# Optimization experiments

Hardware: AMD Instinct MI355X
Metric: run time of the kernel (lower is better)

The kernel has to match this reference:

```python
import jax, jax.numpy as jnp
import numpy as np

N = 100000      # node_size
R = 2000        # rel_size
E = 300000      # triple_size == nnz(adj)
ER = 300000     # nnz of node-to-rel adjacency
EE = 300000     # nnz of node-to-node adjacency
NODE_F = 128
REL_F = 128
ENT_F = NODE_F + REL_F  # 256
DEPTH = 2


def setup_inputs() -> dict:
    key = jax.random.key(0)
    ks = jax.random.split(key, 14)
    return {
        'ent_emb': jax.random.normal(ks[0], (N, NODE_F), jnp.float32) * 0.1,
        'rel_emb': jax.random.normal(ks[1], (R, REL_F), jnp.float32) * 0.1,
        'a_self': jax.random.normal(ks[2], (ENT_F, 1), jnp.float32) * 0.1,
        'a_neigh': jax.random.normal(ks[3], (ENT_F, 1), jnp.float32) * 0.1,
        'a_rel': jax.random.normal(ks[4], (REL_F, 1), jnp.float32) * 0.1,
        'sp_val': jax.random.uniform(ks[5], (E,), jnp.float32),
        'adj_row': jax.random.randint(ks[6], (E,), 0, N),
        'adj_col': jax.random.randint(ks[7], (E,), 0, N),
        'sp_row': jnp.arange(E),
        'sp_col': jax.random.randint(ks[8], (E,), 0, R),
        'rel_row': jax.random.randint(ks[9], (ER,), 0, N),
        'rel_col': jax.random.randint(ks[10], (ER,), 0, R),
        'ent_row': jax.random.randint(ks[11], (EE,), 0, N),
        'ent_col': jax.random.randint(ks[12], (EE,), 0, N),
    }


def _mean_agg(row, col, emb, nrows):
    # tf.sparse_softmax over all-ones values == 1/deg per row -> row mean
    deg = jax.ops.segment_sum(jnp.ones(row.shape, emb.dtype), row, nrows)
    w = 1.0 / deg[row]
    return jax.ops.segment_sum(w[:, None] * emb[col], row, nrows)


def _segment_softmax(vals, seg, nseg):
    m = jax.ops.segment_max(vals, seg, nseg)
    e = jnp.exp(vals - m[seg])
    s = jax.ops.segment_sum(e, seg, nseg)
    return e / s[seg]


def reference(ent_emb, rel_emb, a_self, a_neigh, a_rel, sp_val,
              adj_row, adj_col, sp_row, sp_col, rel_row, rel_col, ent_row, ent_col):
    # initial features: mean-aggregated entity + relation features
    rel_feat = _mean_agg(rel_row, rel_col, rel_emb, N)
    ent_feat = _mean_agg(ent_row, ent_col, ent_emb, N)
    features = jax.nn.relu(jnp.concatenate([ent_feat, rel_feat], axis=-1))  # [N, ENT_F]
    outputs = [features]

    # per-edge relation attention term: (T,R) sparse @ (rel_emb @ a_rel); constant across depth
    rel_proj = (rel_emb @ a_rel)[:, 0]                               # [R]
    rel_attn = jax.ops.segment_sum(sp_val * rel_proj[sp_col], sp_row, E)  # [E]

    att = None
    for _ in range(DEPTH):
        a_s = (features @ a_self)[:, 0]    # [N]
        a_n = (features @ a_neigh)[:, 0]   # [N]
        att = rel_attn + a_s[adj_row] + a_n[adj_col]          # [E]
        att = jax.nn.leaky_relu(att, negative_slope=0.2)
        att = _segment_softmax(att, adj_row, N)               # row-wise sparse softmax
        features = jax.nn.relu(
            jax.ops.segment_sum(att[:, None] * features[adj_col], adj_row, N))
        outputs.append(features)

    out = jnp.concatenate(outputs, axis=-1)  # [N, ENT_F*(DEPTH+1)]
    return out, att
```

## Files before the change

### kernel.cpp

```cpp
#include <hip/hip_runtime.h>

#define NODE_F 128
#define ENT_F  256
#define LDO    768
#define NEG_INF -3.4e38f


__global__ void count3_k(const int* __restrict__ r0, const int* __restrict__ r1,
                         const int* __restrict__ r2, int E0, int E1, int E2,
                         int* __restrict__ deg3, int N) {
    int i = blockIdx.x * blockDim.x + threadIdx.x;
    int y = blockIdx.y;
    const int* rp = (y == 0) ? r0 : (y == 1) ? r1 : r2;
    int Eg = (y == 0) ? E0 : (y == 1) ? E1 : E2;
    if (i < Eg) atomicAdd(&deg3[(size_t)y * N + rp[i]], 1);
}

__global__ void alloc3_k(const int* __restrict__ deg3, int* __restrict__ tot3,
                         int* __restrict__ start3, int* __restrict__ cur3, int N) {
    int y = blockIdx.y;
    int i = blockIdx.x * blockDim.x + threadIdx.x;
    int lane = threadIdx.x & 63;
    int d = (i < N) ? deg3[(size_t)y * N + i] : 0;
    int v = d;
    #pragma unroll
    for (int o = 1; o < 64; o <<= 1) {
        int t = __shfl_up(v, o);
        if (lane >= o) v += t;
    }
    int wsum = __shfl(v, 63);
    int base = 0;
    if (lane == 63) base = atomicAdd(&tot3[y], wsum);
    base = __shfl(base, 63);
    if (i < N) {
        int st = base + v - d;
        start3[(size_t)y * N + i] = st;
        cur3[(size_t)y * N + i] = st;
    }
}

__global__ void scatter3_k(const int* __restrict__ r0, const int* __restrict__ c0,
                           const int* __restrict__ r1, const int* __restrict__ c1,
                           const int* __restrict__ r2, const int* __restrict__ c2,
                           int E0, int E1, int E2, int* __restrict__ cur3,
                           int* __restrict__ col_adj, int* __restrict__ eid_adj,
                           int* __restrict__ col_ent, int* __restrict__ col_rel,
                           const float* __restrict__ sp_val, const int* __restrict__ sp_col,
                           const float* __restrict__ proj, float* __restrict__ rel_attn_s,
                           int N) {
    int e = blockIdx.x * blockDim.x + threadIdx.x;
    int y = blockIdx.y;
    const int* rp = (y == 0) ? r0 : (y == 1) ? r1 : r2;
    const int* cp = (y == 0) ? c0 : (y == 1) ? c1 : c2;
    int* colp = (y == 0) ? col_adj : (y == 1) ? col_ent : col_rel;
    int Eg = (y == 0) ? E0 : (y == 1) ? E1 : E2;
    if (e >= Eg) return;
    int r = rp[e];
    int pos = atomicAdd(&cur3[(size_t)y * N + r], 1);
    colp[pos] = cp[e];
    if (y == 0) {
        eid_adj[pos] = e;
        rel_attn_s[pos] = sp_val[e] * proj[sp_col[e]];
    }
}

__global__ void rel_proj_k(const float* __restrict__ rel_emb, const float* __restrict__ a_rel,
                           float* __restrict__ proj, int R) {
    int r = blockIdx.x * blockDim.x + threadIdx.x;
    if (r >= R) return;
    float s = 0.0f;
    #pragma unroll 4
    for (int f = 0; f < NODE_F; ++f) s += rel_emb[(size_t)r * NODE_F + f] * a_rel[f];
    proj[r] = s;
}


__global__ void meanagg_fused_k(const int* __restrict__ st_ent, const int* __restrict__ dg_ent,
                                const int* __restrict__ col_ent,
                                const int* __restrict__ st_rel, const int* __restrict__ dg_rel,
                                const int* __restrict__ col_rel,
                                const float* __restrict__ ent_emb, const float* __restrict__ rel_emb,
                                const float* __restrict__ a_self, const float* __restrict__ a_neigh,
                                float* __restrict__ out,
                                float* __restrict__ a_s_out, float* __restrict__ a_n_out, int N) {
    int n = blockIdx.x * (blockDim.x >> 6) + (threadIdx.x >> 6);
    int lane = threadIdx.x & 63;
    if (n >= N) return;

    float2 ea = {0.0f, 0.0f};
    {
        int s = st_ent[n], deg = dg_ent[n];
        int p = 0;
        for (; p + 4 <= deg; p += 4) {
            int c0 = col_ent[s + p], c1 = col_ent[s + p + 1];
            int c2 = col_ent[s + p + 2], c3 = col_ent[s + p + 3];
            float2 v0 = reinterpret_cast<const float2*>(&ent_emb[(size_t)c0 * NODE_F])[lane];
            float2 v1 = reinterpret_cast<const float2*>(&ent_emb[(size_t)c1 * NODE_F])[lane];
            float2 v2 = reinterpret_cast<const float2*>(&ent_emb[(size_t)c2 * NODE_F])[lane];
            float2 v3 = reinterpret_cast<const float2*>(&ent_emb[(size_t)c3 * NODE_F])[lane];
            ea.x += v0.x + v1.x + v2.x + v3.x;
            ea.y += v0.y + v1.y + v2.y + v3.y;
        }
        for (; p < deg; ++p) {
            float2 v = reinterpret_cast<const float2*>(&ent_emb[(size_t)col_ent[s + p] * NODE_F])[lane];
            ea.x += v.x; ea.y += v.y;
        }
        if (deg > 0) { float w = 1.0f / (float)deg; ea.x *= w; ea.y *= w; }
    }

    float2 ra = {0.0f, 0.0f};
    {
        int s = st_rel[n], deg = dg_rel[n];
        int p = 0;
        for (; p + 4 <= deg; p += 4) {
            int c0 = col_rel[s + p], c1 = col_rel[s + p + 1];
            int c2 = col_rel[s + p + 2], c3 = col_rel[s + p + 3];
            float2 v0 = reinterpret_cast<const float2*>(&rel_emb[(size_t)c0 * NODE_F])[lane];
            float2 v1 = reinterpret_cast<const float2*>(&rel_emb[(size_t)c1 * NODE_F])[lane];
            float2 v2 = reinterpret_cast<const float2*>(&rel_emb[(size_t)c2 * NODE_F])[lane];
            float2 v3 = reinterpret_cast<const float2*>(&rel_emb[(size_t)c3 * NODE_F])[lane];
            ra.x += v0.x + v1.x + v2.x + v3.x;
            ra.y += v0.y + v1.y + v2.y + v3.y;
        }
        for (; p < deg; ++p) {
            float2 v = reinterpret_cast<const float2*>(&rel_emb[(size_t)col_rel[s + p] * NODE_F])[lane];
            ra.x += v.x; ra.y += v.y;
        }
        if (deg > 0) { float w = 1.0f / (float)deg; ra.x *= w; ra.y *= w; }
    }

    ea.x = ea.x > 0.0f ? ea.x : 0.0f;  ea.y = ea.y > 0.0f ? ea.y : 0.0f;
    ra.x = ra.x > 0.0f ? ra.x : 0.0f;  ra.y = ra.y > 0.0f ? ra.y : 0.0f;

    reinterpret_cast<float2*>(&out[(size_t)n * LDO])[lane] = ea;
    reinterpret_cast<float2*>(&out[(size_t)n * LDO + NODE_F])[lane] = ra;

    float2 se = reinterpret_cast<const float2*>(a_self)[lane];
    float2 sr = reinterpret_cast<const float2*>(a_self)[64 + lane];
    float2 ne = reinterpret_cast<const float2*>(a_neigh)[lane];
    float2 nr = reinterpret_cast<const float2*>(a_neigh)[64 + lane];
    float ds = ea.x * se.x + ea.y * se.y + ra.x * sr.x + ra.y * sr.y;
    float dn = ea.x * ne.x + ea.y * ne.y + ra.x * nr.x + ra.y * nr.y;
    #pragma unroll
    for (int o = 32; o > 0; o >>= 1) {
        ds += __shfl_xor(ds, o);
        dn += __shfl_xor(dn, o);
    }
    if (lane == 0) { a_s_out[n] = ds; a_n_out[n] = dn; }
}

__global__ void attn_agg_fused_k(const int* __restrict__ st, const int* __restrict__ dg,
                                 const int* __restrict__ col_s, const int* __restrict__ eid_s,
                                 const float* __restrict__ rel_attn_s,
                                 const float* __restrict__ a_s_in, const float* __restrict__ a_n_in,
                                 const float* __restrict__ a_self, const float* __restrict__ a_neigh,
                                 float* __restrict__ a_s_out, float* __restrict__ a_n_out,
                                 float* __restrict__ out, int src, int dst,
                                 float* __restrict__ att_out, int N) {
    int n = blockIdx.x * (blockDim.x >> 6) + (threadIdx.x >> 6);
    int lane = threadIdx.x & 63;
    if (n >= N) return;
    int s = st[n];
    int deg = dg[n];
    float4 acc = {0.0f, 0.0f, 0.0f, 0.0f};

    if (deg > 0) {
        float as_row = a_s_in[n];
        if (deg <= 64) {
            float myv = NEG_INF;
            int mycol = 0;
            if (lane < deg) {
                int p = s + lane;
                mycol = col_s[p];
                float v = rel_attn_s[p] + as_row + a_n_in[mycol];
                myv = v >= 0.0f ? v : 0.2f * v;
            }
            float m = myv;
            #pragma unroll
            for (int o = 32; o > 0; o >>= 1) {
                float x = __shfl_xor(m, o);
                m = x > m ? x : m;
            }
            float ex = (lane < deg) ? __expf(myv - m) : 0.0f;
            float ssum = ex;
            #pragma unroll
            for (int o = 32; o > 0; o >>= 1) ssum += __shfl_xor(ssum, o);
            float myatt = ex / ssum;
            if (att_out && lane < deg) att_out[eid_s[s + lane]] = myatt;

            int p = 0;
            for (; p + 4 <= deg; p += 4) {
                float a0 = __shfl(myatt, p),     a1 = __shfl(myatt, p + 1);
                float a2 = __shfl(myatt, p + 2), a3 = __shfl(myatt, p + 3);
                int c0 = __shfl(mycol, p),     c1 = __shfl(mycol, p + 1);
                int c2 = __shfl(mycol, p + 2), c3 = __shfl(mycol, p + 3);
                float4 v0 = reinterpret_cast<const float4*>(&out[(size_t)c0 * LDO + src])[lane];
                float4 v1 = reinterpret_cast<const float4*>(&out[(size_t)c1 * LDO + src])[lane];
                float4 v2 = reinterpret_cast<const float4*>(&out[(size_t)c2 * LDO + src])[lane];
                float4 v3 = reinterpret_cast<const float4*>(&out[(size_t)c3 * LDO + src])[lane];
                acc.x += a0 * v0.x + a1 * v1.x + a2 * v2.x + a3 * v3.x;
                acc.y += a0 * v0.y + a1 * v1.y + a2 * v2.y + a3 * v3.y;
                acc.z += a0 * v0.z + a1 * v1.z + a2 * v2.z + a3 * v3.z;
                acc.w += a0 * v0.w + a1 * v1.w + a2 * v2.w + a3 * v3.w;
            }
            for (; p < deg; ++p) {
                float a = __shfl(myatt, p);
                int c = __shfl(mycol, p);
                float4 v = reinterpret_cast<const float4*>(&out[(size_t)c * LDO + src])[lane];
                acc.x += a * v.x; acc.y += a * v.y; acc.z += a * v.z; acc.w += a * v.w;
            }
        } else {
            float m = NEG_INF;
            for (int p = s + lane; p < s + deg; p += 64) {
                float v = rel_attn_s[p] + as_row + a_n_in[col_s[p]];
                v = v >= 0.0f ? v : 0.2f * v;
                m = v > m ? v : m;
            }
            #pragma unroll
            for (int o = 32; o > 0; o >>= 1) {
                float x = __shfl_xor(m, o);
                m = x > m ? x : m;
            }
            float ssum = 0.0f;
            for (int p = s + lane; p < s + deg; p += 64) {
                float v = rel_attn_s[p] + as_row + a_n_in[col_s[p]];
                v = v >= 0.0f ? v : 0.2f * v;
                ssum += __expf(v - m);
            }
            #pragma unroll
            for (int o = 32; o > 0; o >>= 1) ssum += __shfl_xor(ssum, o);
            float inv = 1.0f / ssum;
            for (int p = s; p < s + deg; ++p) {
                int c = col_s[p];
                float v = rel_attn_s[p] + as_row + a_n_in[c];
                v = v >= 0.0f ? v : 0.2f * v;
                float a = __expf(v - m) * inv;
                if (att_out && lane == 0) att_out[eid_s[p]] = a;
                float4 fv = reinterpret_cast<const float4*>(&out[(size_t)c * LDO + src])[lane];
                acc.x += a * fv.x; acc.y += a * fv.y; acc.z += a * fv.z; acc.w += a * fv.w;
            }
        }
    }

    acc.x = acc.x > 0.0f ? acc.x : 0.0f;
    acc.y = acc.y > 0.0f ? acc.y : 0.0f;
    acc.z = acc.z > 0.0f ? acc.z : 0.0f;
    acc.w = acc.w > 0.0f ? acc.w : 0.0f;
    reinterpret_cast<float4*>(&out[(size_t)n * LDO + dst])[lane] = acc;

    if (a_s_out) {
        float4 s4 = reinterpret_cast<const float4*>(a_self)[lane];
        float4 n4 = reinterpret_cast<const float4*>(a_neigh)[lane];
        float ds = acc.x * s4.x + acc.y * s4.y + acc.z * s4.z + acc.w * s4.w;
        float dn = acc.x * n4.x + acc.y * n4.y + acc.z * n4.z + acc.w * n4.w;
        #pragma unroll
        for (int o = 32; o > 0; o >>= 1) {
            ds += __shfl_xor(ds, o);
            dn += __shfl_xor(dn, o);
        }
        if (lane == 0) { a_s_out[n] = ds; a_n_out[n] = dn; }
    }
}


extern "C" void kernel_launch(void* const* d_in, const int* in_sizes, int n_in,
                              void* d_out, int out_size, void* d_ws, size_t ws_size,
                              hipStream_t stream) {
    const float* ent_emb = (const float*)d_in[0];
    const float* rel_emb = (const float*)d_in[1];
    const float* a_self  = (const float*)d_in[2];
    const float* a_neigh = (const float*)d_in[3];
    const float* a_rel   = (const float*)d_in[4];
    const float* sp_val  = (const float*)d_in[5];
    const int*   adj_row = (const int*)d_in[6];
    const int*   adj_col = (const int*)d_in[7];
    const int*   sp_col  = (const int*)d_in[9];
    const int*   rel_row = (const int*)d_in[10];
    const int*   rel_col = (const int*)d_in[11];
    const int*   ent_row = (const int*)d_in[12];
    const int*   ent_col = (const int*)d_in[13];

    const int N  = in_sizes[0] / NODE_F;
    const int R  = in_sizes[1] / NODE_F;
    const int E  = in_sizes[5];
    const int ER = in_sizes[10];
    const int EE = in_sizes[12];

    float* out = (float*)d_out;
    float* att_out = out + (size_t)N * LDO;

    const int TB = 256;
    int maxE = E > EE ? E : EE; if (ER > maxE) maxE = ER;

    char* w = (char*)d_ws;
    int* deg3    = (int*)w;  w += (size_t)3 * N * 4;
    int* tot3    = (int*)w;  w += 4 * 4;
    int* start3  = (int*)w;  w += (size_t)3 * N * 4;
    int* cur3    = (int*)w;  w += (size_t)3 * N * 4;
    int* col_adj = (int*)w;  w += (size_t)E * 4;
    int* eid_adj = (int*)w;  w += (size_t)E * 4;
    int* col_ent = (int*)w;  w += (size_t)EE * 4;
    int* col_rel = (int*)w;  w += (size_t)ER * 4;
    float* rel_attn_s = (float*)w;  w += (size_t)E * 4;
    float* proj       = (float*)w;  w += (size_t)R * 4;
    float* a_s0       = (float*)w;  w += (size_t)N * 4;
    float* a_n0       = (float*)w;  w += (size_t)N * 4;
    float* a_s1       = (float*)w;  w += (size_t)N * 4;
    float* a_n1       = (float*)w;  w += (size_t)N * 4;

    int* st_adj = start3;          int* dg_adj = deg3;
    int* st_ent = start3 + N;      int* dg_ent = deg3 + N;
    int* st_rel = start3 + 2 * N;  int* dg_rel = deg3 + 2 * N;

    rel_proj_k<<<(R + TB - 1) / TB, TB, 0, stream>>>(rel_emb, a_rel, proj, R);

    hipMemsetAsync(deg3, 0, ((size_t)3 * N + 4) * sizeof(int), stream);
    {
        dim3 g((maxE + TB - 1) / TB, 3);
        count3_k<<<g, TB, 0, stream>>>(adj_row, ent_row, rel_row, E, EE, ER, deg3, N);
    }
    {
        dim3 g((N + TB - 1) / TB, 3);
        alloc3_k<<<g, TB, 0, stream>>>(deg3, tot3, start3, cur3, N);
    }
    {
        dim3 g((maxE + TB - 1) / TB, 3);
        scatter3_k<<<g, TB, 0, stream>>>(adj_row, adj_col, ent_row, ent_col, rel_row, rel_col,
                                         E, EE, ER, cur3, col_adj, eid_adj, col_ent, col_rel,
                                         sp_val, sp_col, proj, rel_attn_s, N);
    }

    meanagg_fused_k<<<(N + 3) / 4, 256, 0, stream>>>(st_ent, dg_ent, col_ent,
                                                     st_rel, dg_rel, col_rel,
                                                     ent_emb, rel_emb, a_self, a_neigh,
                                                     out, a_s0, a_n0, N);

    attn_agg_fused_k<<<(N + 3) / 4, 256, 0, stream>>>(st_adj, dg_adj, col_adj, eid_adj,
                                                      rel_attn_s, a_s0, a_n0, a_self, a_neigh,
                                                      a_s1, a_n1, out, 0, ENT_F, nullptr, N);

    attn_agg_fused_k<<<(N + 3) / 4, 256, 0, stream>>>(st_adj, dg_adj, col_adj, eid_adj,
                                                      rel_attn_s, a_s1, a_n1, nullptr, nullptr,
                                                      nullptr, nullptr, out, ENT_F, 2 * ENT_F,
                                                      att_out, N);
}
```

Baseline: 388.0 us.

## Split edge attention logits into separate edge-parallel kernel and add nontemporal stores

Moves the per-edge leaky-relu attention logit computation out of the per-node aggregation kernel into a new edge-parallel kernel. It writes logits to a CSR-ordered buffer, using a new row_adj array recorded during the scatter. The aggregation kernel then reads precomputed logits instead of gathering a_n and recomputing them, which avoids the repeated recomputation for high-degree rows. The final layer also uses nontemporal stores for the output features and attention. The cost is two extra kernel launches and extra global traffic for the logit buffer.

```diff
diff --git a/kernel.cpp b/kernel.cpp
--- a/kernel.cpp
+++ b/kernel.cpp
@@ -4,6 +4,8 @@
 #define ENT_F  256
 #define LDO    768
 #define NEG_INF -3.4e38f
+
+typedef float vf4 __attribute__((ext_vector_type(4)));
 
 
 __global__ void count3_k(const int* __restrict__ r0, const int* __restrict__ r1,
@@ -44,6 +46,7 @@
                            const int* __restrict__ r2, const int* __restrict__ c2,
                            int E0, int E1, int E2, int* __restrict__ cur3,
                            int* __restrict__ col_adj, int* __restrict__ eid_adj,
+                           int* __restrict__ row_adj,
                            int* __restrict__ col_ent, int* __restrict__ col_rel,
                            const float* __restrict__ sp_val, const int* __restrict__ sp_col,
                            const float* __restrict__ proj, float* __restrict__ rel_attn_s,
@@ -60,6 +63,7 @@
     colp[pos] = cp[e];
     if (y == 0) {
         eid_adj[pos] = e;
+        row_adj[pos] = r;
         rel_attn_s[pos] = sp_val[e] * proj[sp_col[e]];
     }
 }
@@ -72,6 +76,16 @@
     #pragma unroll 4
     for (int f = 0; f < NODE_F; ++f) s += rel_emb[(size_t)r * NODE_F + f] * a_rel[f];
     proj[r] = s;
+}
+
+__global__ void edge_att_k(const int* __restrict__ row_s, const int* __restrict__ col_s,
+                           const float* __restrict__ rel_attn_s,
+                           const float* __restrict__ a_s, const float* __restrict__ a_n,
+                           float* __restrict__ att_raw, int E) {
+    int p = blockIdx.x * blockDim.x + threadIdx.x;
+    if (p >= E) return;
+    float v = rel_attn_s[p] + a_s[row_s[p]] + a_n[col_s[p]];
+    att_raw[p] = v >= 0.0f ? v : 0.2f * v;
 }
 
 
@@ -149,14 +163,14 @@
     if (lane == 0) { a_s_out[n] = ds; a_n_out[n] = dn; }
 }
 
-__global__ void attn_agg_fused_k(const int* __restrict__ st, const int* __restrict__ dg,
-                                 const int* __restrict__ col_s, const int* __restrict__ eid_s,
-                                 const float* __restrict__ rel_attn_s,
-                                 const float* __restrict__ a_s_in, const float* __restrict__ a_n_in,
-                                 const float* __restrict__ a_self, const float* __restrict__ a_neigh,
-                                 float* __restrict__ a_s_out, float* __restrict__ a_n_out,
-                                 float* __restrict__ out, int src, int dst,
-                                 float* __restrict__ att_out, int N) {
+template <int NT>
+__global__ void attn_agg_slim_k(const int* __restrict__ st, const int* __restrict__ dg,
+                                const int* __restrict__ col_s, const int* __restrict__ eid_s,
+                                const float* __restrict__ att_raw,
+                                const float* __restrict__ a_self, const float* __restrict__ a_neigh,
+                                float* __restrict__ a_s_out, float* __restrict__ a_n_out,
+                                float* __restrict__ out, int src, int dst,
+                                float* __restrict__ att_out, int N) {
     int n = blockIdx.x * (blockDim.x >> 6) + (threadIdx.x >> 6);
     int lane = threadIdx.x & 63;
     if (n >= N) return;
@@ -165,15 +179,12 @@
     float4 acc = {0.0f, 0.0f, 0.0f, 0.0f};
 
     if (deg > 0) {
-        float as_row = a_s_in[n];
         if (deg <= 64) {
             float myv = NEG_INF;
             int mycol = 0;
             if (lane < deg) {
-                int p = s + lane;
-                mycol = col_s[p];
-                float v = rel_attn_s[p] + as_row + a_n_in[mycol];
-                myv = v >= 0.0f ? v : 0.2f * v;
+                mycol = col_s[s + lane];
+                myv = att_raw[s + lane];
             }
             float m = myv;
             #pragma unroll
@@ -186,7 +197,10 @@
             #pragma unroll
             for (int o = 32; o > 0; o >>= 1) ssum += __shfl_xor(ssum, o);
             float myatt = ex / ssum;
-            if (att_out && lane < deg) att_out[eid_s[s + lane]] = myatt;
+            if (att_out && lane < deg) {
+                if (NT) __builtin_nontemporal_store(myatt, &att_out[eid_s[s + lane]]);
+                else    att_out[eid_s[s + lane]] = myatt;
+            }
 
             int p = 0;
             for (; p + 4 <= deg; p += 4) {
@@ -212,8 +226,7 @@
         } else {
             float m = NEG_INF;
             for (int p = s + lane; p < s + deg; p += 64) {
-                float v = rel_attn_s[p] + as_row + a_n_in[col_s[p]];
-                v = v >= 0.0f ? v : 0.2f * v;
+                float v = att_raw[p];
                 m = v > m ? v : m;
             }
             #pragma unroll
@@ -222,19 +235,13 @@
                 m = x > m ? x : m;
             }
             float ssum = 0.0f;
-            for (int p = s + lane; p < s + deg; p += 64) {
-                float v = rel_attn_s[p] + as_row + a_n_in[col_s[p]];
-                v = v >= 0.0f ? v : 0.2f * v;
-                ssum += __expf(v - m);
-            }
+            for (int p = s + lane; p < s + deg; p += 64) ssum += __expf(att_raw[p] - m);
             #pragma unroll
             for (int o = 32; o > 0; o >>= 1) ssum += __shfl_xor(ssum, o);
             float inv = 1.0f / ssum;
             for (int p = s; p < s + deg; ++p) {
                 int c = col_s[p];
-                float v = rel_attn_s[p] + as_row + a_n_in[c];
-                v = v >= 0.0f ? v : 0.2f * v;
-                float a = __expf(v - m) * inv;
+                float a = __expf(att_raw[p] - m) * inv;
                 if (att_out && lane == 0) att_out[eid_s[p]] = a;
                 float4 fv = reinterpret_cast<const float4*>(&out[(size_t)c * LDO + src])[lane];
                 acc.x += a * fv.x; acc.y += a * fv.y; acc.z += a * fv.z; acc.w += a * fv.w;
@@ -246,7 +253,13 @@
     acc.y = acc.y > 0.0f ? acc.y : 0.0f;
     acc.z = acc.z > 0.0f ? acc.z : 0.0f;
     acc.w = acc.w > 0.0f ? acc.w : 0.0f;
-    reinterpret_cast<float4*>(&out[(size_t)n * LDO + dst])[lane] = acc;
+    float* dstp = &out[(size_t)n * LDO + dst] + (size_t)lane * 4;
+    if (NT) {
+        vf4 v; v.x = acc.x; v.y = acc.y; v.z = acc.z; v.w = acc.w;
+        __builtin_nontemporal_store(v, reinterpret_cast<vf4*>(dstp));
+    } else {
+        *reinterpret_cast<float4*>(dstp) = acc;
+    }
 
     if (a_s_out) {
         float4 s4 = reinterpret_cast<const float4*>(a_self)[lane];
@@ -299,9 +312,11 @@
     int* cur3    = (int*)w;  w += (size_t)3 * N * 4;
     int* col_adj = (int*)w;  w += (size_t)E * 4;
     int* eid_adj = (int*)w;  w += (size_t)E * 4;
+    int* row_adj = (int*)w;  w += (size_t)E * 4;
     int* col_ent = (int*)w;  w += (size_t)EE * 4;
     int* col_rel = (int*)w;  w += (size_t)ER * 4;
     float* rel_attn_s = (float*)w;  w += (size_t)E * 4;
+    float* att_raw    = (float*)w;  w += (size_t)E * 4;
     float* proj       = (float*)w;  w += (size_t)R * 4;
     float* a_s0       = (float*)w;  w += (size_t)N * 4;
     float* a_n0       = (float*)w;  w += (size_t)N * 4;
@@ -312,6 +327,8 @@
     int* st_ent = start3 + N;      int* dg_ent = deg3 + N;
     int* st_rel = start3 + 2 * N;  int* dg_rel = deg3 + 2 * N;
 
+    const int gE = (E + TB - 1) / TB;
+
     rel_proj_k<<<(R + TB - 1) / TB, TB, 0, stream>>>(rel_emb, a_rel, proj, R);
 
     hipMemsetAsync(deg3, 0, ((size_t)3 * N + 4) * sizeof(int), stream);
@@ -326,8 +343,8 @@
     {
         dim3 g((maxE + TB - 1) / TB, 3);
         scatter3_k<<<g, TB, 0, stream>>>(adj_row, adj_col, ent_row, ent_col, rel_row, rel_col,
-                                         E, EE, ER, cur3, col_adj, eid_adj, col_ent, col_rel,
-                                         sp_val, sp_col, proj, rel_attn_s, N);
+                                         E, EE, ER, cur3, col_adj, eid_adj, row_adj,
+                                         col_ent, col_rel, sp_val, sp_col, proj, rel_attn_s, N);
     }
 
     meanagg_fused_k<<<(N + 3) / 4, 256, 0, stream>>>(st_ent, dg_ent, col_ent,
@@ -335,12 +352,13 @@
                                                      ent_emb, rel_emb, a_self, a_neigh,
                                                      out, a_s0, a_n0, N);
 
-    attn_agg_fused_k<<<(N + 3) / 4, 256, 0, stream>>>(st_adj, dg_adj, col_adj, eid_adj,
-                                                      rel_attn_s, a_s0, a_n0, a_self, a_neigh,
-                                                      a_s1, a_n1, out, 0, ENT_F, nullptr, N);
-
-    attn_agg_fused_k<<<(N + 3) / 4, 256, 0, stream>>>(st_adj, dg_adj, col_adj, eid_adj,
-                                                      rel_attn_s, a_s1, a_n1, nullptr, nullptr,
-                                                      nullptr, nullptr, out, ENT_F, 2 * ENT_F,
-                                                      att_out, N);
-}
+    edge_att_k<<<gE, TB, 0, stream>>>(row_adj, col_adj, rel_attn_s, a_s0, a_n0, att_raw, E);
+    attn_agg_slim_k<0><<<(N + 3) / 4, 256, 0, stream>>>(st_adj, dg_adj, col_adj, eid_adj,
+                                                        att_raw, a_self, a_neigh, a_s1, a_n1,
+                                                        out, 0, ENT_F, nullptr, N);
+
+    edge_att_k<<<gE, TB, 0, stream>>>(row_adj, col_adj, rel_attn_s, a_s1, a_n1, att_raw, E);
+    attn_agg_slim_k<1><<<(N + 3) / 4, 256, 0, stream>>>(st_adj, dg_adj, col_adj, eid_adj,
+                                                        att_raw, nullptr, nullptr, nullptr, nullptr,
+                                                        out, ENT_F, 2 * ENT_F, att_out, N);
+}
```

New measurement: 378.5 us. 1.03x faster.
